# Optimization experiments

Measured on AMD Instinct MI355X. Metric: run time of the kernel, lower is better.

The kernel has to match this reference:

```python
import jax, jax.numpy as jnp
import numpy as np
from jax import lax

DIM = 128
HEADS = 8
B, H, W = 8, 128, 128


def conv1x1(w, x):
    # w: [out_c, in_c], x: [b, in_c, h, w]
    return jnp.einsum('oc,bchw->bohw', w, x)


def setup_inputs() -> dict:
    key = jax.random.key(0)
    ks = jax.random.split(key, 12)
    s = 0.02
    return {
        'x': jax.random.normal(ks[0], (B, DIM, H, W), dtype=jnp.float32),
        'W_qkv': jax.random.normal(ks[1], (3 * DIM, DIM), dtype=jnp.float32) * s,
        'W_dw': jax.random.normal(ks[2], (DIM, 1, 3, 3), dtype=jnp.float32) * s,
        'W_proj_s': jax.random.normal(ks[3], (DIM, DIM), dtype=jnp.float32) * s,
        'scale_s': jnp.ones((HEADS, 1, 1), dtype=jnp.float32),
        'W_ff1': jax.random.normal(ks[4], (DIM, DIM), dtype=jnp.float32) * s,
        'W_ff2': jax.random.normal(ks[5], (DIM, DIM), dtype=jnp.float32) * s,
        'W_proj_f': jax.random.normal(ks[6], (DIM, DIM), dtype=jnp.float32) * s,
        'W_gsf': jax.random.normal(ks[7], (DIM, DIM), dtype=jnp.float32) * s,
        'b_gsf': jnp.zeros((DIM,), dtype=jnp.float32),
        'W_gfs': jax.random.normal(ks[8], (DIM, DIM), dtype=jnp.float32) * s,
        'b_gfs': jnp.zeros((DIM,), dtype=jnp.float32),
    }


def reference(x, W_qkv, W_dw, W_proj_s, scale_s, W_ff1, W_ff2, W_proj_f,
              W_gsf, b_gsf, W_gfs, b_gfs):
    b, c, h, w = x.shape
    head = HEADS
    ch = c // head

    # --- channel self-attention branch ---
    qkv = conv1x1(W_qkv, x)                      # [b, 3c, h, w]
    q_s, k_s, v_s = jnp.split(qkv, 3, axis=1)
    v_s_conv = lax.conv_general_dilated(
        v_s, W_dw, window_strides=(1, 1), padding='SAME',
        feature_group_count=c,
        dimension_numbers=('NCHW', 'OIHW', 'NCHW'))  # depthwise 3x3

    q = q_s.reshape(b, head, ch, h * w)
    k = k_s.reshape(b, head, ch, h * w)
    v = v_s.reshape(b, head, ch, h * w)
    attn = jax.nn.softmax(jnp.einsum('bhcn,bhdn->bhcd', q, k) * scale_s, axis=-1)
    out_s = jnp.einsum('bhcd,bhdn->bhcn', attn, v).reshape(b, c, h, w)
    out_s = conv1x1(W_proj_s, out_s + v_s_conv)

    # --- frequency filter branch ---
    xf = jnp.fft.rfft2(x, norm='ortho')          # complex [b,c,h,w//2+1]
    spatial_weights = conv1x1(W_ff2, jax.nn.gelu(conv1x1(W_ff1, x), approximate=False))
    freq_weights = jnp.fft.rfft2(spatial_weights, norm='ortho')
    out_f = jnp.fft.irfft2(xf * freq_weights, s=(h, w), norm='ortho')
    out_f = conv1x1(W_proj_f, out_f)

    # --- sigmoid-gated fusion ---
    gate_f = jax.nn.sigmoid(conv1x1(W_gsf, out_s) + b_gsf[:, None, None])
    gate_s = jax.nn.sigmoid(conv1x1(W_gfs, out_f) + b_gfs[:, None, None])
    return x + out_s * gate_s + out_f * gate_f
```

## Files before the change

### kernel.cpp

```cpp
#include <hip/hip_runtime.h>
#include <hip/hip_bf16.h>
#include <math.h>

#define HW 16384

typedef __attribute__((ext_vector_type(8))) short bf16x8;
typedef __attribute__((ext_vector_type(4))) float f32x4;

__device__ __forceinline__ unsigned short f2bf(float a)
{
    __hip_bfloat16 h = __float2bfloat16(a);
    return __builtin_bit_cast(unsigned short, h);
}
__device__ __forceinline__ unsigned f2bf_pk(float a, float b)
{
    return (unsigned)f2bf(a) | ((unsigned)f2bf(b) << 16);
}
__device__ __forceinline__ float bf2f(unsigned short u)
{
    return __uint_as_float(((unsigned)u) << 16);
}
__device__ __forceinline__ float sigmoidf_(float v) { return 1.f / (1.f + expf(-v)); }

__device__ __forceinline__ float2 cmul(float2 a, float2 b)
{
    return make_float2(a.x * b.x - a.y * b.y, a.x * b.y + a.y * b.x);
}

__global__ __launch_bounds__(256)
void wprep_k(const float* __restrict__ w0, const float* __restrict__ w1,
             const float* __restrict__ w2, const float* __restrict__ w3,
             const float* __restrict__ w4, const float* __restrict__ w5,
             const float* __restrict__ w6, int4* __restrict__ Wbf4)
{
    int m = blockIdx.x >> 3;
    int slot = (blockIdx.x & 7) * 256 + threadIdx.x;
    const float* src;
    switch (m) {
        case 0: src = w0; break;
        case 1: src = w1; break;
        case 2: src = w2; break;
        case 3: src = w3; break;
        case 4: src = w4; break;
        case 5: src = w5; break;
        default: src = w6; break;
    }
    int o = slot >> 4;
    int c16 = (slot & 15) ^ (o & 7);
    const float* p = src + o * 128 + c16 * 8;
    int4 pk;
    pk.x = f2bf_pk(p[0], p[1]); pk.y = f2bf_pk(p[2], p[3]);
    pk.z = f2bf_pk(p[4], p[5]); pk.w = f2bf_pk(p[6], p[7]);
    Wbf4[m * 2048 + slot] = pk;
}

__global__ __launch_bounds__(256)
void head_k(const float* __restrict__ x, const int4* __restrict__ wv,
            const int4* __restrict__ w1, const int4* __restrict__ w2,
            unsigned short* __restrict__ V, unsigned short* __restrict__ swb)
{
    __shared__ short WL[128 * 128];
    __shared__ short XLx[64 * 128];
    __shared__ short XM[64 * 128];
    int t = threadIdx.x;
    int gb = blockIdx.x;
    int b = gb >> 8;
    int n0 = (gb & 255) << 6;

    #pragma unroll
    for (int it = 0; it < 8; ++it)
        ((int4*)WL)[it * 256 + t] = wv[it * 256 + t];

    const float* inb = x + (size_t)b * 128 * HW + n0;
    int nl = t & 63;
    #pragma unroll
    for (int it = 0; it < 4; ++it) {
        int c8 = (t >> 6) + it * 4;
        float v[8];
        #pragma unroll
        for (int j = 0; j < 8; ++j) v[j] = inb[(size_t)(c8 * 8 + j) * HW + nl];
        int4 p;
        p.x = f2bf_pk(v[0], v[1]); p.y = f2bf_pk(v[2], v[3]);
        p.z = f2bf_pk(v[4], v[5]); p.w = f2bf_pk(v[6], v[7]);
        ((int4*)XLx)[nl * 16 + (c8 ^ (nl & 7))] = p;
    }
    __syncthreads();

    int l = t & 63, w = t >> 6, kg = l >> 4, l15 = l & 15, l7 = l15 & 7;

    f32x4 acc[2][4];
    #pragma unroll
    for (int mf = 0; mf < 2; ++mf)
        #pragma unroll
        for (int nf = 0; nf < 4; ++nf) acc[mf][nf] = (f32x4){0.f, 0.f, 0.f, 0.f};
    #pragma unroll
    for (int ks = 0; ks < 4; ++ks) {
        int ch = ks * 4 + kg;
        bf16x8 A0 = ((const bf16x8*)WL)[(w * 32 + l15) * 16 + (ch ^ l7)];
        bf16x8 A1 = ((const bf16x8*)WL)[(w * 32 + 16 + l15) * 16 + (ch ^ l7)];
        #pragma unroll
        for (int nf = 0; nf < 4; ++nf) {
            bf16x8 Bf = ((const bf16x8*)XLx)[(nf * 16 + l15) * 16 + (ch ^ l7)];
            acc[0][nf] = __builtin_amdgcn_mfma_f32_16x16x32_bf16(A0, Bf, acc[0][nf], 0, 0, 0);
            acc[1][nf] = __builtin_amdgcn_mfma_f32_16x16x32_bf16(A1, Bf, acc[1][nf], 0, 0, 0);
        }
    }
    #pragma unroll
    for (int mf = 0; mf < 2; ++mf)
        #pragma unroll
        for (int nf = 0; nf < 4; ++nf)
            #pragma unroll
            for (int i = 0; i < 4; ++i) {
                int row = w * 32 + mf * 16 + kg * 4 + i;
                int col = n0 + nf * 16 + l15;
                V[((size_t)b * 128 + row) * HW + col] = f2bf(acc[mf][nf][i]);
            }
    __syncthreads();

    #pragma unroll
    for (int it = 0; it < 8; ++it)
        ((int4*)WL)[it * 256 + t] = w1[it * 256 + t];
    __syncthreads();

    #pragma unroll
    for (int mf = 0; mf < 2; ++mf)
        #pragma unroll
        for (int nf = 0; nf < 4; ++nf) acc[mf][nf] = (f32x4){0.f, 0.f, 0.f, 0.f};
    #pragma unroll
    for (int ks = 0; ks < 4; ++ks) {
        int ch = ks * 4 + kg;
        bf16x8 A0 = ((const bf16x8*)WL)[(w * 32 + l15) * 16 + (ch ^ l7)];
        bf16x8 A1 = ((const bf16x8*)WL)[(w * 32 + 16 + l15) * 16 + (ch ^ l7)];
        #pragma unroll
        for (int nf = 0; nf < 4; ++nf) {
            bf16x8 Bf = ((const bf16x8*)XLx)[(nf * 16 + l15) * 16 + (ch ^ l7)];
            acc[0][nf] = __builtin_amdgcn_mfma_f32_16x16x32_bf16(A0, Bf, acc[0][nf], 0, 0, 0);
            acc[1][nf] = __builtin_amdgcn_mfma_f32_16x16x32_bf16(A1, Bf, acc[1][nf], 0, 0, 0);
        }
    }
    __syncthreads();

    #pragma unroll
    for (int it = 0; it < 8; ++it)
        ((int4*)WL)[it * 256 + t] = w2[it * 256 + t];
    #pragma unroll
    for (int mf = 0; mf < 2; ++mf)
        #pragma unroll
        for (int nf = 0; nf < 4; ++nf) {
            float g4[4];
            #pragma unroll
            for (int i = 0; i < 4; ++i) {
                float v = acc[mf][nf][i];
                g4[i] = 0.5f * v * (1.0f + erff(v * 0.70710678118654752f));
            }
            int col = nf * 16 + l15;
            int r0 = w * 32 + mf * 16 + kg * 4;
            int octet = r0 >> 3;
            uint2 pk2;
            pk2.x = f2bf_pk(g4[0], g4[1]);
            pk2.y = f2bf_pk(g4[2], g4[3]);
            ((uint2*)XM)[(col * 16 + (octet ^ (col & 7))) * 2 + (kg & 1)] = pk2;
        }
    __syncthreads();

    f32x4 acc2[2][4];
    #pragma unroll
    for (int mf = 0; mf < 2; ++mf)
        #pragma unroll
        for (int nf = 0; nf < 4; ++nf) acc2[mf][nf] = (f32x4){0.f, 0.f, 0.f, 0.f};
    #pragma unroll
    for (int ks = 0; ks < 4; ++ks) {
        int ch = ks * 4 + kg;
        bf16x8 A0 = ((const bf16x8*)WL)[(w * 32 + l15) * 16 + (ch ^ l7)];
        bf16x8 A1 = ((const bf16x8*)WL)[(w * 32 + 16 + l15) * 16 + (ch ^ l7)];
        #pragma unroll
        for (int nf = 0; nf < 4; ++nf) {
            bf16x8 Bf = ((const bf16x8*)XM)[(nf * 16 + l15) * 16 + (ch ^ l7)];
            acc2[0][nf] = __builtin_amdgcn_mfma_f32_16x16x32_bf16(A0, Bf, acc2[0][nf], 0, 0, 0);
            acc2[1][nf] = __builtin_amdgcn_mfma_f32_16x16x32_bf16(A1, Bf, acc2[1][nf], 0, 0, 0);
        }
    }
    #pragma unroll
    for (int mf = 0; mf < 2; ++mf)
        #pragma unroll
        for (int nf = 0; nf < 4; ++nf)
            #pragma unroll
            for (int i = 0; i < 4; ++i) {
                int row = w * 32 + mf * 16 + kg * 4 + i;
                int col = n0 + nf * 16 + l15;
                swb[((size_t)b * 128 + row) * HW + col] = f2bf(acc2[mf][nf][i]);
            }
}

__global__ __launch_bounds__(256)
void dwconv_k(const unsigned short* __restrict__ V, const float* __restrict__ Wdw,
              unsigned short* __restrict__ vcb)
{
    int tid = blockIdx.x * 256 + threadIdx.x;
    int e4 = tid & 4095;
    int bc = tid >> 12;
    int c = bc & 127;
    int y = e4 >> 5;
    int x0 = (e4 & 31) << 2;
    const unsigned short* vin = V + (size_t)bc * HW;
    float wf[9];
    #pragma unroll
    for (int i = 0; i < 9; ++i) wf[i] = Wdw[c * 9 + i];
    float a0 = 0.f, a1 = 0.f, a2 = 0.f, a3 = 0.f;
    #pragma unroll
    for (int dy = 0; dy < 3; ++dy) {
        int yy = y + dy - 1;
        if (yy < 0 || yy > 127) continue;
        const unsigned short* r = vin + yy * 128;
        uint2 mu = *(const uint2*)(r + x0);
        float m0 = bf2f((unsigned short)(mu.x & 0xFFFF));
        float m1 = bf2f((unsigned short)(mu.x >> 16));
        float m2 = bf2f((unsigned short)(mu.y & 0xFFFF));
        float m3 = bf2f((unsigned short)(mu.y >> 16));
        float left  = (x0 > 0)   ? bf2f(r[x0 - 1]) : 0.f;
        float right = (x0 < 124) ? bf2f(r[x0 + 4]) : 0.f;
        float w0 = wf[dy * 3], w1 = wf[dy * 3 + 1], w2 = wf[dy * 3 + 2];
        a0 += w0 * left + w1 * m0 + w2 * m1;
        a1 += w0 * m0   + w1 * m1 + w2 * m2;
        a2 += w0 * m1   + w1 * m2 + w2 * m3;
        a3 += w0 * m2   + w1 * m3 + w2 * right;
    }
    uint2 r2;
    r2.x = f2bf_pk(a0, a1);
    r2.y = f2bf_pk(a2, a3);
    *(uint2*)(vcb + (size_t)bc * HW + y * 128 + x0) = r2;
}

__global__ __launch_bounds__(256)
void gram_mfma_k(const float* __restrict__ x, float* __restrict__ Gp)
{
    __shared__ short XL[128 * 128];
    int t = threadIdx.x;
    int blk = blockIdx.x;
    int b = blk >> 5, ks = blk & 31;
    const float* xb = x + (size_t)b * 128 * HW + ks * 512;
    int l = t & 63, w = t >> 6, kg = l >> 4, l15 = l & 15, l7 = l15 & 7;

    f32x4 acc[2][8];
    #pragma unroll
    for (int mf = 0; mf < 2; ++mf)
        #pragma unroll
        for (int nf = 0; nf < 8; ++nf) acc[mf][nf] = (f32x4){0.f, 0.f, 0.f, 0.f};

    for (int kc = 0; kc < 4; ++kc) {
        __syncthreads();
        #pragma unroll
        for (int it = 0; it < 8; ++it) {
            int g = it * 256 + t;
            int row = g >> 4, oct = g & 15;
            const float* p = xb + (size_t)row * HW + kc * 128 + oct * 8;
            int4 pk;
            pk.x = f2bf_pk(p[0], p[1]); pk.y = f2bf_pk(p[2], p[3]);
            pk.z = f2bf_pk(p[4], p[5]); pk.w = f2bf_pk(p[6], p[7]);
            ((int4*)XL)[row * 16 + (oct ^ (row & 7))] = pk;
        }
        __syncthreads();
        #pragma unroll
        for (int s = 0; s < 4; ++s) {
            int oct = s * 4 + kg;
            bf16x8 A0 = ((const bf16x8*)XL)[(w * 32 + l15) * 16 + (oct ^ l7)];
            bf16x8 A1 = ((const bf16x8*)XL)[(w * 32 + 16 + l15) * 16 + (oct ^ l7)];
            #pragma unroll
            for (int nf = 0; nf < 8; ++nf) {
                bf16x8 Bf = ((const bf16x8*)XL)[(nf * 16 + l15) * 16 + (oct ^ l7)];
                acc[0][nf] = __builtin_amdgcn_mfma_f32_16x16x32_bf16(A0, Bf, acc[0][nf], 0, 0, 0);
                acc[1][nf] = __builtin_amdgcn_mfma_f32_16x16x32_bf16(A1, Bf, acc[1][nf], 0, 0, 0);
            }
        }
    }
    float* gp = Gp + (size_t)blk * 16384;
    #pragma unroll
    for (int mf = 0; mf < 2; ++mf)
        #pragma unroll
        for (int nf = 0; nf < 8; ++nf)
            #pragma unroll
            for (int i = 0; i < 4; ++i) {
                int row = w * 32 + mf * 16 + kg * 4 + i;
                int col = nf * 16 + l15;
                gp[row * 128 + col] = acc[mf][nf][i];
            }
}

__global__ void gram_reduce_k(const float* __restrict__ Gp, float* __restrict__ G)
{
    int idx = blockIdx.x * 256 + threadIdx.x;
    int b = idx >> 14;
    int ij = idx & 16383;
    const float* gp = Gp + (size_t)(b * 32) * 16384 + ij;
    float s = 0.f;
    #pragma unroll
    for (int ks = 0; ks < 32; ++ks) s += gp[(size_t)ks * 16384];
    G[idx] = s;
}

__global__ __launch_bounds__(256)
void attn_s2_k(const float* __restrict__ G, const float* __restrict__ Wqkv,
               const float* __restrict__ scale, float* __restrict__ S)
{
    __shared__ float Wq[16][129];
    __shared__ float Wk[16][129];
    __shared__ float Ts[16][129];
    int bh = blockIdx.x;
    int b = bh >> 3, h = bh & 7;
    int t = threadIdx.x;
    #pragma unroll
    for (int i = 0; i < 8; ++i) {
        int idx = t + i * 256;
        int r = idx >> 7, ci = idx & 127;
        Wq[r][ci] = Wqkv[(size_t)(h * 16 + r) * 128 + ci];
        Wk[r][ci] = Wqkv[(size_t)(128 + h * 16 + r) * 128 + ci];
    }
    __syncthreads();
    const float* Gb = G + (size_t)b * 16384;
    #pragma unroll
    for (int i = 0; i < 8; ++i) {
        int idx = t + i * 256;
        int c = idx >> 7, col = idx & 127;
        float s = 0.f;
        #pragma unroll 8
        for (int ci = 0; ci < 128; ++ci)
            s += Wq[c][ci] * Gb[ci * 128 + col];
        Ts[c][col] = s;
    }
    __syncthreads();
    int c = t >> 4, d = t & 15;
    float s = 0.f;
    #pragma unroll 8
    for (int col = 0; col < 128; ++col)
        s += Ts[c][col] * Wk[d][col];
    s *= scale[h];
    float m = s;
    #pragma unroll
    for (int w = 1; w < 16; w <<= 1)
        m = fmaxf(m, __shfl_xor(m, w, 64));
    float e = expf(s - m);
    float sum = e;
    #pragma unroll
    for (int w = 1; w < 16; w <<= 1)
        sum += __shfl_xor(sum, w, 64);
    S[(size_t)bh * 256 + t] = e / sum;
}

__global__ __launch_bounds__(256)
void proj_s_pv_k(const unsigned short* __restrict__ V,
                 const unsigned short* __restrict__ vcb,
                 const float* __restrict__ S, const int4* __restrict__ wbf,
                 unsigned short* __restrict__ out_s)
{
    __shared__ short WL[128 * 128];
    __shared__ short XL[64 * 128];
    __shared__ float SL[2048];
    int t = threadIdx.x;
    int gb = blockIdx.x;
    int b = gb >> 8;
    int n0 = (gb & 255) << 6;

    #pragma unroll
    for (int it = 0; it < 8; ++it)
        ((int4*)WL)[it * 256 + t] = wbf[it * 256 + t];
    #pragma unroll
    for (int i = 0; i < 8; ++i)
        SL[i * 256 + t] = S[(size_t)b * 2048 + i * 256 + t];
    __syncthreads();

    int col = t & 63, w = t >> 6;
    #pragma unroll
    for (int hh = 0; hh < 2; ++hh) {
        int h = w * 2 + hh;
        float v[16];
        #pragma unroll
        for (int d = 0; d < 16; ++d)
            v[d] = bf2f(V[((size_t)(b * 128 + h * 16 + d)) * HW + n0 + col]);
        float o[16];
        #pragma unroll
        for (int c = 0; c < 16; ++c) {
            const float* sl = SL + h * 256 + c * 16;
            float s = 0.f;
            #pragma unroll
            for (int d = 0; d < 16; ++d) s += sl[d] * v[d];
            o[c] = s + bf2f(vcb[((size_t)(b * 128 + h * 16 + c)) * HW + n0 + col]);
        }
        #pragma unroll
        for (int oc = 0; oc < 2; ++oc) {
            int octet = h * 2 + oc;
            int4 p;
            p.x = f2bf_pk(o[oc * 8 + 0], o[oc * 8 + 1]);
            p.y = f2bf_pk(o[oc * 8 + 2], o[oc * 8 + 3]);
            p.z = f2bf_pk(o[oc * 8 + 4], o[oc * 8 + 5]);
            p.w = f2bf_pk(o[oc * 8 + 6], o[oc * 8 + 7]);
            ((int4*)XL)[col * 16 + (octet ^ (col & 7))] = p;
        }
    }
    __syncthreads();

    int l = t & 63, kg = l >> 4, l15 = l & 15, l7 = l15 & 7;
    f32x4 acc[2][4];
    #pragma unroll
    for (int mf = 0; mf < 2; ++mf)
        #pragma unroll
        for (int nf = 0; nf < 4; ++nf) acc[mf][nf] = (f32x4){0.f, 0.f, 0.f, 0.f};
    #pragma unroll
    for (int ks = 0; ks < 4; ++ks) {
        int ch = ks * 4 + kg;
        bf16x8 A0 = ((const bf16x8*)WL)[(w * 32 + l15) * 16 + (ch ^ l7)];
        bf16x8 A1 = ((const bf16x8*)WL)[(w * 32 + 16 + l15) * 16 + (ch ^ l7)];
        #pragma unroll
        for (int nf = 0; nf < 4; ++nf) {
            bf16x8 Bf = ((const bf16x8*)XL)[(nf * 16 + l15) * 16 + (ch ^ l7)];
            acc[0][nf] = __builtin_amdgcn_mfma_f32_16x16x32_bf16(A0, Bf, acc[0][nf], 0, 0, 0);
            acc[1][nf] = __builtin_amdgcn_mfma_f32_16x16x32_bf16(A1, Bf, acc[1][nf], 0, 0, 0);
        }
    }
    #pragma unroll
    for (int mf = 0; mf < 2; ++mf)
        #pragma unroll
        for (int nf = 0; nf < 4; ++nf)
            #pragma unroll
            for (int i = 0; i < 4; ++i) {
                int row = w * 32 + mf * 16 + kg * 4 + i;
                int colg = n0 + nf * 16 + l15;
                out_s[((size_t)b * 128 + row) * HW + colg] = f2bf(acc[mf][nf][i]);
            }
}

__global__ __launch_bounds__(256)
void tail_k(const float* __restrict__ x, const unsigned short* __restrict__ outs,
            const unsigned short* __restrict__ pre,
            const int4* __restrict__ wpf,
            const int4* __restrict__ wgsf, const float* __restrict__ bgsf,
            const int4* __restrict__ wgfs, const float* __restrict__ bgfs,
            float* __restrict__ out)
{
    __shared__ short WL[128 * 128];
    __shared__ short XP[64 * 128];
    __shared__ short XS[64 * 128];
    int t = threadIdx.x;
    int gb = blockIdx.x;
    int T = (gb & 7) * 256 + (gb >> 3);
    int b = T >> 8;
    int n0 = (T & 255) << 6;

    #pragma unroll
    for (int it = 0; it < 8; ++it)
        ((int4*)WL)[it * 256 + t] = wpf[it * 256 + t];

    const unsigned short* pb = pre + (size_t)b * 128 * HW + n0;
    const unsigned short* sb = outs + (size_t)b * 128 * HW + n0;
    int nl = t & 63;
    #pragma unroll
    for (int it = 0; it < 4; ++it) {
        int c8 = (t >> 6) + it * 4;
        unsigned up[8], us[8];
        #pragma unroll
        for (int j = 0; j < 8; ++j) {
            size_t a = (size_t)(c8 * 8 + j) * HW + nl;
            up[j] = pb[a];
            us[j] = sb[a];
        }
        int4 pp, ps;
        pp.x = (int)(up[0] | (up[1] << 16)); pp.y = (int)(up[2] | (up[3] << 16));
        pp.z = (int)(up[4] | (up[5] << 16)); pp.w = (int)(up[6] | (up[7] << 16));
        ps.x = (int)(us[0] | (us[1] << 16)); ps.y = (int)(us[2] | (us[3] << 16));
        ps.z = (int)(us[4] | (us[5] << 16)); ps.w = (int)(us[6] | (us[7] << 16));
        ((int4*)XP)[nl * 16 + (c8 ^ (nl & 7))] = pp;
        ((int4*)XS)[nl * 16 + (c8 ^ (nl & 7))] = ps;
    }
    __syncthreads();

    int l = t & 63, w = t >> 6, kg = l >> 4, l15 = l & 15, l7 = l15 & 7;

    f32x4 accF[2][4];
    #pragma unroll
    for (int mf = 0; mf < 2; ++mf)
        #pragma unroll
        for (int nf = 0; nf < 4; ++nf) accF[mf][nf] = (f32x4){0.f, 0.f, 0.f, 0.f};
    #pragma unroll
    for (int ks = 0; ks < 4; ++ks) {
        int ch = ks * 4 + kg;
        bf16x8 A0 = ((const bf16x8*)WL)[(w * 32 + l15) * 16 + (ch ^ l7)];
        bf16x8 A1 = ((const bf16x8*)WL)[(w * 32 + 16 + l15) * 16 + (ch ^ l7)];
        #pragma unroll
        for (int nf = 0; nf < 4; ++nf) {
            bf16x8 Bf = ((const bf16x8*)XP)[(nf * 16 + l15) * 16 + (ch ^ l7)];
            accF[0][nf] = __builtin_amdgcn_mfma_f32_16x16x32_bf16(A0, Bf, accF[0][nf], 0, 0, 0);
            accF[1][nf] = __builtin_amdgcn_mfma_f32_16x16x32_bf16(A1, Bf, accF[1][nf], 0, 0, 0);
        }
    }
    __syncthreads();

    #pragma unroll
    for (int it = 0; it < 8; ++it)
        ((int4*)WL)[it * 256 + t] = wgsf[it * 256 + t];
    #pragma unroll
    for (int mf = 0; mf < 2; ++mf)
        #pragma unroll
        for (int nf = 0; nf < 4; ++nf) {
            int col = nf * 16 + l15;
            int r0 = w * 32 + mf * 16 + kg * 4;
            int octet = r0 >> 3;
            uint2 pk2;
            pk2.x = f2bf_pk(accF[mf][nf][0], accF[mf][nf][1]);
            pk2.y = f2bf_pk(accF[mf][nf][2], accF[mf][nf][3]);
            ((uint2*)XP)[(col * 16 + (octet ^ (col & 7))) * 2 + (kg & 1)] = pk2;
        }
    __syncthreads();

    f32x4 aS[2][4];
    #pragma unroll
    for (int mf = 0; mf < 2; ++mf)
        #pragma unroll
        for (int nf = 0; nf < 4; ++nf) aS[mf][nf] = (f32x4){0.f, 0.f, 0.f, 0.f};
    #pragma unroll
    for (int ks = 0; ks < 4; ++ks) {
        int ch = ks * 4 + kg;
        bf16x8 A0 = ((const bf16x8*)WL)[(w * 32 + l15) * 16 + (ch ^ l7)];
        bf16x8 A1 = ((const bf16x8*)WL)[(w * 32 + 16 + l15) * 16 + (ch ^ l7)];
        #pragma unroll
        for (int nf = 0; nf < 4; ++nf) {
            bf16x8 Bf = ((const bf16x8*)XS)[(nf * 16 + l15) * 16 + (ch ^ l7)];
            aS[0][nf] = __builtin_amdgcn_mfma_f32_16x16x32_bf16(A0, Bf, aS[0][nf], 0, 0, 0);
            aS[1][nf] = __builtin_amdgcn_mfma_f32_16x16x32_bf16(A1, Bf, aS[1][nf], 0, 0, 0);
        }
    }
    __syncthreads();

    #pragma unroll
    for (int it = 0; it < 8; ++it)
        ((int4*)WL)[it * 256 + t] = wgfs[it * 256 + t];
    __syncthreads();

    f32x4 aF[2][4];
    #pragma unroll
    for (int mf = 0; mf < 2; ++mf)
        #pragma unroll
        for (int nf = 0; nf < 4; ++nf) aF[mf][nf] = (f32x4){0.f, 0.f, 0.f, 0.f};
    #pragma unroll
    for (int ks = 0; ks < 4; ++ks) {
        int ch = ks * 4 + kg;
        bf16x8 A0 = ((const bf16x8*)WL)[(w * 32 + l15) * 16 + (ch ^ l7)];
        bf16x8 A1 = ((const bf16x8*)WL)[(w * 32 + 16 + l15) * 16 + (ch ^ l7)];
        #pragma unroll
        for (int nf = 0; nf < 4; ++nf) {
            bf16x8 Bf = ((const bf16x8*)XP)[(nf * 16 + l15) * 16 + (ch ^ l7)];
            aF[0][nf] = __builtin_amdgcn_mfma_f32_16x16x32_bf16(A0, Bf, aF[0][nf], 0, 0, 0);
            aF[1][nf] = __builtin_amdgcn_mfma_f32_16x16x32_bf16(A1, Bf, aF[1][nf], 0, 0, 0);
        }
    }

    #pragma unroll
    for (int mf = 0; mf < 2; ++mf)
        #pragma unroll
        for (int nf = 0; nf < 4; ++nf)
            #pragma unroll
            for (int i = 0; i < 4; ++i) {
                int row = w * 32 + mf * 16 + kg * 4 + i;
                int cc = n0 + nf * 16 + l15;
                float gf = sigmoidf_(aS[mf][nf][i] + bgsf[row]);
                float gs = sigmoidf_(aF[mf][nf][i] + bgfs[row]);
                size_t gi = ((size_t)(b * 128) + row) * HW + cc;
                float os = bf2f(outs[gi]);
                float of = accF[mf][nf][i];
                out[gi] = x[gi] + os * gs + of * gf;
            }
}

__device__ __forceinline__ int ZIX(int r, int j)
{
    return r * 128 + (j ^ (((r ^ (r >> 4)) & 3) << 3) ^ (((j >> 4) & 3) << 1));
}
__device__ __forceinline__ float2 zld(const unsigned* Z, int r, int j)
{
    unsigned z = Z[ZIX(r, j)];
    return make_float2(bf2f((unsigned short)(z & 0xFFFF)),
                       bf2f((unsigned short)(z >> 16)));
}
__device__ __forceinline__ void zst(unsigned* Z, int r, int j, float2 v)
{
    Z[ZIX(r, j)] = f2bf_pk(v.x, v.y);
}

__device__ __forceinline__ void dft16(float2* v)
{
    const float C1 = 0.92387953251f, S1 = 0.38268343236f, R2 = 0.70710678119f;
    const float2 W16[8] = {
        {1.f, 0.f}, {C1, -S1}, {R2, -R2}, {S1, -C1},
        {0.f, -1.f}, {-S1, -C1}, {-R2, -R2}, {-C1, -S1}};
    #pragma unroll
    for (int i = 0; i < 8; ++i) {
        float2 a = v[i], b = v[i + 8];
        v[i] = make_float2(a.x + b.x, a.y + b.y);
        float2 d = make_float2(a.x - b.x, a.y - b.y);
        v[i + 8] = cmul(d, W16[i]);
    }
    #pragma unroll
    for (int blk = 0; blk < 16; blk += 8)
        #pragma unroll
        for (int i = 0; i < 4; ++i) {
            float2 a = v[blk + i], b = v[blk + i + 4];
            v[blk + i] = make_float2(a.x + b.x, a.y + b.y);
            float2 d = make_float2(a.x - b.x, a.y - b.y);
            v[blk + i + 4] = cmul(d, W16[2 * i]);
        }
    #pragma unroll
    for (int blk = 0; blk < 16; blk += 4) {
        float2 a0 = v[blk], b0 = v[blk + 2];
        v[blk] = make_float2(a0.x + b0.x, a0.y + b0.y);
        v[blk + 2] = make_float2(a0.x - b0.x, a0.y - b0.y);
        float2 a1 = v[blk + 1], b1 = v[blk + 3];
        v[blk + 1] = make_float2(a1.x + b1.x, a1.y + b1.y);
        float2 d = make_float2(a1.x - b1.x, a1.y - b1.y);
        v[blk + 3] = make_float2(d.y, -d.x);
    }
    #pragma unroll
    for (int blk = 0; blk < 16; blk += 2) {
        float2 a = v[blk], b = v[blk + 1];
        v[blk] = make_float2(a.x + b.x, a.y + b.y);
        v[blk + 1] = make_float2(a.x - b.x, a.y - b.y);
    }
}

__device__ __forceinline__ void dft8(float2* v)
{
    const float R2 = 0.70710678119f;
    const float2 W8[4] = {{1.f, 0.f}, {R2, -R2}, {0.f, -1.f}, {-R2, -R2}};
    #pragma unroll
    for (int i = 0; i < 4; ++i) {
        float2 a = v[i], b = v[i + 4];
        v[i] = make_float2(a.x + b.x, a.y + b.y);
        float2 d = make_float2(a.x - b.x, a.y - b.y);
        v[i + 4] = cmul(d, W8[i]);
    }
    #pragma unroll
    for (int blk = 0; blk < 8; blk += 4) {
        float2 a0 = v[blk], b0 = v[blk + 2];
        v[blk] = make_float2(a0.x + b0.x, a0.y + b0.y);
        v[blk + 2] = make_float2(a0.x - b0.x, a0.y - b0.y);
        float2 a1 = v[blk + 1], b1 = v[blk + 3];
        v[blk + 1] = make_float2(a1.x + b1.x, a1.y + b1.y);
        float2 d = make_float2(a1.x - b1.x, a1.y - b1.y);
        v[blk + 3] = make_float2(d.y, -d.x);
    }
    #pragma unroll
    for (int blk = 0; blk < 8; blk += 2) {
        float2 a = v[blk], b = v[blk + 1];
        v[blk] = make_float2(a.x + b.x, a.y + b.y);
        v[blk + 1] = make_float2(a.x - b.x, a.y - b.y);
    }
}

__device__ __forceinline__ void fft_line_row(unsigned* Z, const float2* tw,
                                             int row, int n2)
{
    const int BREV4[16] = {0,8,4,12,2,10,6,14,1,9,5,13,3,11,7,15};
    const int BREV3[8] = {0,4,2,6,1,5,3,7};
    float2 v[16];
    #pragma unroll
    for (int n1 = 0; n1 < 16; ++n1) v[n1] = zld(Z, row, 8 * n1 + n2);
    dft16(v);
    #pragma unroll
    for (int p = 0; p < 16; ++p) {
        int k1 = BREV4[p];
        zst(Z, row, 16 * n2 + k1, cmul(v[p], tw[n2 * k1]));
    }
    float2 wa[8], wb[8];
    #pragma unroll
    for (int m = 0; m < 8; ++m) {
        wa[m] = zld(Z, row, 16 * m + n2);
        wb[m] = zld(Z, row, 16 * m + n2 + 8);
    }
    dft8(wa);
    dft8(wb);
    #pragma unroll
    for (int p = 0; p < 8; ++p) {
        zst(Z, row, n2 + 16 * BREV3[p], wa[p]);
        zst(Z, row, n2 + 8 + 16 * BREV3[p], wb[p]);
    }
}

__device__ __forceinline__ void fft_line_col(unsigned* Z, const float2* tw,
                                             int col, int n2)
{
    const int BREV4[16] = {0,8,4,12,2,10,6,14,1,9,5,13,3,11,7,15};
    const int BREV3[8] = {0,4,2,6,1,5,3,7};
    float2 v[16];
    #pragma unroll
    for (int n1 = 0; n1 < 16; ++n1) v[n1] = zld(Z, 8 * n1 + n2, col);
    dft16(v);
    #pragma unroll
    for (int p = 0; p < 16; ++p) {
        int k1 = BREV4[p];
        zst(Z, 16 * n2 + k1, col, cmul(v[p], tw[n2 * k1]));
    }
    float2 wa[8], wb[8];
    #pragma unroll
    for (int m = 0; m < 8; ++m) {
        wa[m] = zld(Z, 16 * m + n2, col);
        wb[m] = zld(Z, 16 * m + n2 + 8, col);
    }
    dft8(wa);
    dft8(wb);
    #pragma unroll
    for (int p = 0; p < 8; ++p) {
        zst(Z, n2 + 16 * BREV3[p], col, wa[p]);
        zst(Z, n2 + 8 + 16 * BREV3[p], col, wb[p]);
    }
}

__global__ __launch_bounds__(256)
void fft_all_k(const float* __restrict__ x, const unsigned short* __restrict__ sw,
               unsigned short* __restrict__ outp)
{
    __shared__ unsigned Z[128 * 128];
    __shared__ float2 tw[128];
    const int BREV3[8] = {0,4,2,6,1,5,3,7};
    int t = threadIdx.x;
    if (t < 128) {
        float sn, cs;
        sincosf(0.049087385212340519f * (float)t, &sn, &cs);
        tw[t] = make_float2(cs, -sn);
    }
    size_t base = (size_t)blockIdx.x * HW;

    #pragma unroll
    for (int i = 0; i < 64; ++i) {
        int idx = t + i * 256;
        int r = idx >> 7, j = idx & 127;
        Z[ZIX(r, j)] = (unsigned)f2bf(x[base + idx]) |
                       ((unsigned)sw[base + idx] << 16);
    }
    __syncthreads();

    int ln = t >> 3, n2 = t & 7;
    #pragma unroll
    for (int it = 0; it < 4; ++it) fft_line_row(Z, tw, it * 32 + ln, n2);
    __syncthreads();
    #pragma unroll
    for (int it = 0; it < 4; ++it) fft_line_col(Z, tw, it * 32 + ln, n2);
    __syncthreads();

    for (int item = t; item < 8194; item += 256) {
        int rA, kA, rB, kB;
        if (item < 8064) {
            rA = 1 + (item >> 7); kA = item & 127;
            rB = 128 - rA; kB = (128 - kA) & 127;
        } else {
            int it2 = item - 8064;
            rA = rB = (it2 < 65) ? 0 : 64;
            kA = (it2 < 65) ? it2 : (it2 - 65);
            kB = (128 - kA) & 127;
        }
        float2 z1 = zld(Z, rA, kA);
        float2 z2 = zld(Z, rB, kB);
        float2 X = make_float2(0.5f * (z1.x + z2.x), 0.5f * (z1.y - z2.y));
        float Dx = z1.x - z2.x, Dy = z1.y + z2.y;
        float2 Wf = make_float2(0.5f * Dy, -0.5f * Dx);
        float2 Y = cmul(X, Wf);
        zst(Z, rA, kA, make_float2(Y.x, -Y.y));
        zst(Z, rB, kB, Y);
    }
    __syncthreads();

    #pragma unroll
    for (int it = 0; it < 4; ++it) fft_line_col(Z, tw, it * 32 + ln, n2);
    __syncthreads();

    const float scale = 1.f / 2097152.f;
    const int BREV4[16] = {0,8,4,12,2,10,6,14,1,9,5,13,3,11,7,15};
    #pragma unroll
    for (int it = 0; it < 4; ++it) {
        int row = it * 32 + ln;
        float2 v[16];
        #pragma unroll
        for (int n1 = 0; n1 < 16; ++n1) v[n1] = zld(Z, row, 8 * n1 + n2);
        dft16(v);
        #pragma unroll
        for (int p = 0; p < 16; ++p) {
            int k1 = BREV4[p];
            zst(Z, row, 16 * n2 + k1, cmul(v[p], tw[n2 * k1]));
        }
        float2 wa[8], wb[8];
        #pragma unroll
        for (int m = 0; m < 8; ++m) {
            wa[m] = zld(Z, row, 16 * m + n2);
            wb[m] = zld(Z, row, 16 * m + n2 + 8);
        }
        dft8(wa);
        dft8(wb);
        #pragma unroll
        for (int p = 0; p < 8; ++p) {
            outp[base + row * 128 + n2 + 16 * BREV3[p]] = f2bf(wa[p].x * scale);
            outp[base + row * 128 + n2 + 8 + 16 * BREV3[p]] = f2bf(wb[p].x * scale);
        }
    }
}

extern "C" void kernel_launch(void* const* d_in, const int* in_sizes, int n_in,
                              void* d_out, int out_size, void* d_ws, size_t ws_size,
                              hipStream_t stream)
{
    const float* x        = (const float*)d_in[0];
    const float* W_qkv    = (const float*)d_in[1];
    const float* W_dw     = (const float*)d_in[2];
    const float* W_proj_s = (const float*)d_in[3];
    const float* scale_s  = (const float*)d_in[4];
    const float* W_ff1    = (const float*)d_in[5];
    const float* W_ff2    = (const float*)d_in[6];
    const float* W_proj_f = (const float*)d_in[7];
    const float* W_gsf    = (const float*)d_in[8];
    const float* b_gsf    = (const float*)d_in[9];
    const float* W_gfs    = (const float*)d_in[10];
    const float* b_gfs    = (const float*)d_in[11];
    float* out = (float*)d_out;

    char* ws = (char*)d_ws;
    const size_t MB32 = 33554432ull;
    const size_t MB64 = 67108864ull;
    const size_t MB96 = 100663296ull;
    unsigned short* V     = (unsigned short*)(ws);
    unsigned short* out_s = (unsigned short*)(ws + MB32);
    unsigned short* swb   = (unsigned short*)(ws + MB64);
    unsigned short* pre   = (unsigned short*)(ws + MB64);
    int4* Wbf4            = (int4*)(ws + MB96);
    unsigned short* vcb   = (unsigned short*)out;
    float* Gp  = out + 8388608;
    float* G   = out + 8388608 + 4194304;
    float* S   = G + 131072;

    wprep_k<<<56, 256, 0, stream>>>(W_qkv + 256 * 128, W_proj_s, W_ff1, W_ff2,
                                    W_proj_f, W_gsf, W_gfs, Wbf4);

    head_k<<<2048, 256, 0, stream>>>(x, Wbf4 + 0 * 2048, Wbf4 + 2 * 2048,
                                     Wbf4 + 3 * 2048, V, swb);

    dwconv_k<<<16384, 256, 0, stream>>>(V, W_dw, vcb);
    gram_mfma_k<<<256, 256, 0, stream>>>(x, Gp);
    gram_reduce_k<<<512, 256, 0, stream>>>(Gp, G);
    attn_s2_k<<<64, 256, 0, stream>>>(G, W_qkv, scale_s, S);
    proj_s_pv_k<<<2048, 256, 0, stream>>>(V, vcb, S, Wbf4 + 1 * 2048, out_s);

    fft_all_k<<<1024, 256, 0, stream>>>(x, swb, pre);

    tail_k<<<2048, 256, 0, stream>>>(x, out_s, pre, Wbf4 + 4 * 2048,
                                     Wbf4 + 5 * 2048, b_gsf,
                                     Wbf4 + 6 * 2048, b_gfs, out);
}
```

Measured before the change: 300.4 us.

## Cache bf16 copy of x in head kernel and tile dwconv through LDS

```diff
diff --git a/kernel.cpp b/kernel.cpp
--- a/kernel.cpp
+++ b/kernel.cpp
@@ -57,7 +57,8 @@
 __global__ __launch_bounds__(256)
 void head_k(const float* __restrict__ x, const int4* __restrict__ wv,
             const int4* __restrict__ w1, const int4* __restrict__ w2,
-            unsigned short* __restrict__ V, unsigned short* __restrict__ swb)
+            unsigned short* __restrict__ V, unsigned short* __restrict__ swb,
+            unsigned short* __restrict__ xb)
 {
     __shared__ short WL[128 * 128];
     __shared__ short XLx[64 * 128];
@@ -77,11 +78,18 @@
     for (int it = 0; it < 4; ++it) {
         int c8 = (t >> 6) + it * 4;
         float v[8];
-        #pragma unroll
-        for (int j = 0; j < 8; ++j) v[j] = inb[(size_t)(c8 * 8 + j) * HW + nl];
+        unsigned short vb[8];
+        #pragma unroll
+        for (int j = 0; j < 8; ++j) {
+            v[j] = inb[(size_t)(c8 * 8 + j) * HW + nl];
+            vb[j] = f2bf(v[j]);
+            xb[((size_t)(b * 128) + c8 * 8 + j) * HW + n0 + nl] = vb[j];
+        }
         int4 p;
-        p.x = f2bf_pk(v[0], v[1]); p.y = f2bf_pk(v[2], v[3]);
-        p.z = f2bf_pk(v[4], v[5]); p.w = f2bf_pk(v[6], v[7]);
+        p.x = (int)((unsigned)vb[0] | ((unsigned)vb[1] << 16));
+        p.y = (int)((unsigned)vb[2] | ((unsigned)vb[3] << 16));
+        p.z = (int)((unsigned)vb[4] | ((unsigned)vb[5] << 16));
+        p.w = (int)((unsigned)vb[6] | ((unsigned)vb[7] << 16));
         ((int4*)XLx)[nl * 16 + (c8 ^ (nl & 7))] = p;
     }
     __syncthreads();
@@ -196,49 +204,59 @@
 void dwconv_k(const unsigned short* __restrict__ V, const float* __restrict__ Wdw,
               unsigned short* __restrict__ vcb)
 {
-    int tid = blockIdx.x * 256 + threadIdx.x;
-    int e4 = tid & 4095;
-    int bc = tid >> 12;
+    __shared__ unsigned short Vt[128 * 128];
+    int t = threadIdx.x;
+    int bc = blockIdx.x;
     int c = bc & 127;
-    int y = e4 >> 5;
-    int x0 = (e4 & 31) << 2;
     const unsigned short* vin = V + (size_t)bc * HW;
+    #pragma unroll
+    for (int i = 0; i < 16; ++i) {
+        int idx = i * 256 + t;
+        ((uint2*)Vt)[idx] = ((const uint2*)vin)[idx];
+    }
     float wf[9];
     #pragma unroll
     for (int i = 0; i < 9; ++i) wf[i] = Wdw[c * 9 + i];
-    float a0 = 0.f, a1 = 0.f, a2 = 0.f, a3 = 0.f;
-    #pragma unroll
-    for (int dy = 0; dy < 3; ++dy) {
-        int yy = y + dy - 1;
-        if (yy < 0 || yy > 127) continue;
-        const unsigned short* r = vin + yy * 128;
-        uint2 mu = *(const uint2*)(r + x0);
-        float m0 = bf2f((unsigned short)(mu.x & 0xFFFF));
-        float m1 = bf2f((unsigned short)(mu.x >> 16));
-        float m2 = bf2f((unsigned short)(mu.y & 0xFFFF));
-        float m3 = bf2f((unsigned short)(mu.y >> 16));
-        float left  = (x0 > 0)   ? bf2f(r[x0 - 1]) : 0.f;
-        float right = (x0 < 124) ? bf2f(r[x0 + 4]) : 0.f;
-        float w0 = wf[dy * 3], w1 = wf[dy * 3 + 1], w2 = wf[dy * 3 + 2];
-        a0 += w0 * left + w1 * m0 + w2 * m1;
-        a1 += w0 * m0   + w1 * m1 + w2 * m2;
-        a2 += w0 * m1   + w1 * m2 + w2 * m3;
-        a3 += w0 * m2   + w1 * m3 + w2 * right;
-    }
-    uint2 r2;
-    r2.x = f2bf_pk(a0, a1);
-    r2.y = f2bf_pk(a2, a3);
-    *(uint2*)(vcb + (size_t)bc * HW + y * 128 + x0) = r2;
+    __syncthreads();
+    #pragma unroll
+    for (int i = 0; i < 16; ++i) {
+        int q = i * 256 + t;
+        int y = q >> 5;
+        int x0 = (q & 31) << 2;
+        float a0 = 0.f, a1 = 0.f, a2 = 0.f, a3 = 0.f;
+        #pragma unroll
+        for (int dy = 0; dy < 3; ++dy) {
+            int yy = y + dy - 1;
+            if (yy < 0 || yy > 127) continue;
+            const unsigned short* r = Vt + yy * 128;
+            uint2 mu = *(const uint2*)(r + x0);
+            float m0 = bf2f((unsigned short)(mu.x & 0xFFFF));
+            float m1 = bf2f((unsigned short)(mu.x >> 16));
+            float m2 = bf2f((unsigned short)(mu.y & 0xFFFF));
+            float m3 = bf2f((unsigned short)(mu.y >> 16));
+            float left  = (x0 > 0)   ? bf2f(r[x0 - 1]) : 0.f;
+            float right = (x0 < 124) ? bf2f(r[x0 + 4]) : 0.f;
+            float w0 = wf[dy * 3], w1 = wf[dy * 3 + 1], w2 = wf[dy * 3 + 2];
+            a0 += w0 * left + w1 * m0 + w2 * m1;
+            a1 += w0 * m0   + w1 * m1 + w2 * m2;
+            a2 += w0 * m1   + w1 * m2 + w2 * m3;
+            a3 += w0 * m2   + w1 * m3 + w2 * right;
+        }
+        uint2 r2;
+        r2.x = f2bf_pk(a0, a1);
+        r2.y = f2bf_pk(a2, a3);
+        *(uint2*)(vcb + (size_t)bc * HW + y * 128 + x0) = r2;
+    }
 }
 
 __global__ __launch_bounds__(256)
-void gram_mfma_k(const float* __restrict__ x, float* __restrict__ Gp)
+void gram_mfma_k(const unsigned short* __restrict__ xb, float* __restrict__ Gp)
 {
     __shared__ short XL[128 * 128];
     int t = threadIdx.x;
     int blk = blockIdx.x;
     int b = blk >> 5, ks = blk & 31;
-    const float* xb = x + (size_t)b * 128 * HW + ks * 512;
+    const unsigned short* xbb = xb + (size_t)b * 128 * HW + ks * 512;
     int l = t & 63, w = t >> 6, kg = l >> 4, l15 = l & 15, l7 = l15 & 7;
 
     f32x4 acc[2][8];
@@ -253,11 +271,8 @@
         for (int it = 0; it < 8; ++it) {
             int g = it * 256 + t;
             int row = g >> 4, oct = g & 15;
-            const float* p = xb + (size_t)row * HW + kc * 128 + oct * 8;
-            int4 pk;
-            pk.x = f2bf_pk(p[0], p[1]); pk.y = f2bf_pk(p[2], p[3]);
-            pk.z = f2bf_pk(p[4], p[5]); pk.w = f2bf_pk(p[6], p[7]);
-            ((int4*)XL)[row * 16 + (oct ^ (row & 7))] = pk;
+            ((int4*)XL)[row * 16 + (oct ^ (row & 7))] =
+                *(const int4*)(xbb + (size_t)row * HW + kc * 128 + oct * 8);
         }
         __syncthreads();
         #pragma unroll
@@ -712,7 +727,8 @@
 }
 
 __global__ __launch_bounds__(256)
-void fft_all_k(const float* __restrict__ x, const unsigned short* __restrict__ sw,
+void fft_all_k(const unsigned short* __restrict__ xb,
+               const unsigned short* __restrict__ sw,
                unsigned short* __restrict__ outp)
 {
     __shared__ unsigned Z[128 * 128];
@@ -727,11 +743,15 @@
     size_t base = (size_t)blockIdx.x * HW;
 
     #pragma unroll
-    for (int i = 0; i < 64; ++i) {
-        int idx = t + i * 256;
-        int r = idx >> 7, j = idx & 127;
-        Z[ZIX(r, j)] = (unsigned)f2bf(x[base + idx]) |
-                       ((unsigned)sw[base + idx] << 16);
+    for (int i = 0; i < 16; ++i) {
+        int idx4 = (i * 256 + t) * 4;
+        int r = idx4 >> 7, j = idx4 & 127;
+        uint2 xv = *(const uint2*)(xb + base + idx4);
+        uint2 sv = *(const uint2*)(sw + base + idx4);
+        Z[ZIX(r, j + 0)] = (xv.x & 0xFFFFu) | (sv.x << 16);
+        Z[ZIX(r, j + 1)] = (xv.x >> 16)     | (sv.x & 0xFFFF0000u);
+        Z[ZIX(r, j + 2)] = (xv.y & 0xFFFFu) | (sv.y << 16);
+        Z[ZIX(r, j + 3)] = (xv.y >> 16)     | (sv.y & 0xFFFF0000u);
     }
     __syncthreads();
 
@@ -821,29 +841,31 @@
     const size_t MB32 = 33554432ull;
     const size_t MB64 = 67108864ull;
     const size_t MB96 = 100663296ull;
+    const size_t MB97 = 101711872ull;
     unsigned short* V     = (unsigned short*)(ws);
     unsigned short* out_s = (unsigned short*)(ws + MB32);
     unsigned short* swb   = (unsigned short*)(ws + MB64);
     unsigned short* pre   = (unsigned short*)(ws + MB64);
     int4* Wbf4            = (int4*)(ws + MB96);
-    unsigned short* vcb   = (unsigned short*)out;
-    float* Gp  = out + 8388608;
-    float* G   = out + 8388608 + 4194304;
+    float* Gp  = (float*)(ws + MB97);
+    float* G   = Gp + 4194304;
     float* S   = G + 131072;
+    unsigned short* vcb = (unsigned short*)out;
+    unsigned short* xb  = (unsigned short*)out + 16777216;
 
     wprep_k<<<56, 256, 0, stream>>>(W_qkv + 256 * 128, W_proj_s, W_ff1, W_ff2,
                                     W_proj_f, W_gsf, W_gfs, Wbf4);
 
     head_k<<<2048, 256, 0, stream>>>(x, Wbf4 + 0 * 2048, Wbf4 + 2 * 2048,
-                                     Wbf4 + 3 * 2048, V, swb);
-
-    dwconv_k<<<16384, 256, 0, stream>>>(V, W_dw, vcb);
-    gram_mfma_k<<<256, 256, 0, stream>>>(x, Gp);
+                                     Wbf4 + 3 * 2048, V, swb, xb);
+
+    dwconv_k<<<1024, 256, 0, stream>>>(V, W_dw, vcb);
+    gram_mfma_k<<<256, 256, 0, stream>>>(xb, Gp);
     gram_reduce_k<<<512, 256, 0, stream>>>(Gp, G);
     attn_s2_k<<<64, 256, 0, stream>>>(G, W_qkv, scale_s, S);
     proj_s_pv_k<<<2048, 256, 0, stream>>>(V, vcb, S, Wbf4 + 1 * 2048, out_s);
 
-    fft_all_k<<<1024, 256, 0, stream>>>(x, swb, pre);
+    fft_all_k<<<1024, 256, 0, stream>>>(xb, swb, pre);
 
     tail_k<<<2048, 256, 0, stream>>>(x, out_s, pre, Wbf4 + 4 * 2048,
                                      Wbf4 + 5 * 2048, b_gsf,
```

After: 286.0 us (median of 2 runs). -4.8%, faster.
